# Kernel optimization log

Measured on AMD Instinct MI355X. Metric: run time of the kernel, lower is better.

Reference implementation:

```python
import jax, jax.numpy as jnp
import numpy as np

B, N = 1, 768
C_A, C_S, C_Z = 768, 384, 128
H, C_HID, N_TRANS = 16, 48, 2
INF = 1e9
PNAMES = ['attn_s_ln_g', 'attn_ada_gate_w', 'attn_ada_gate_b', 'attn_ada_skip_w',
          'wq', 'bq', 'wk', 'wv', 'z_ln_g', 'z_ln_b', 'wb', 'wg', 'wo',
          'attn_out_gate_w', 'attn_out_gate_b',
          'tr_s_ln_g', 'tr_ada_gate_w', 'tr_ada_gate_b', 'tr_ada_skip_w',
          'tr_w1', 'tr_w2', 'tr_wo', 'tr_out_gate_w', 'tr_out_gate_b']


def _ln(x, eps=1e-5):
    mu = jnp.mean(x, axis=-1, keepdims=True)
    var = jnp.mean((x - mu) ** 2, axis=-1, keepdims=True)
    return (x - mu) * jax.lax.rsqrt(var + eps)


def _adaln(a, s, s_g, gate_w, gate_b, skip_w):
    # AF3 Algorithm 26 AdaLN: a <- LN(a, no affine); s <- LN(s, scale only)
    a_ln = _ln(a)
    s_ln = _ln(s) * s_g
    return jax.nn.sigmoid(s_ln @ gate_w + gate_b) * a_ln + s_ln @ skip_w


def setup_inputs() -> dict:
    key = jax.random.key(0)
    ks = iter(jax.random.split(key, 40))
    w = lambda *sh: jax.random.normal(next(ks), sh, jnp.float32) * 0.02
    return dict(
        a=jax.random.normal(next(ks), (B, N, C_A), jnp.float32),
        s=jax.random.normal(next(ks), (B, N, C_S), jnp.float32),
        z=jax.random.normal(next(ks), (B, N, N, C_Z), jnp.float32),
        mask=jnp.ones((B, N), jnp.int32),
        attn_s_ln_g=jnp.ones((C_S,), jnp.float32),
        attn_ada_gate_w=w(C_S, C_A),
        attn_ada_gate_b=jnp.zeros((C_A,), jnp.float32),
        attn_ada_skip_w=w(C_S, C_A),
        wq=w(C_A, H * C_HID), bq=jnp.zeros((H * C_HID,), jnp.float32),
        wk=w(C_A, H * C_HID), wv=w(C_A, H * C_HID),
        z_ln_g=jnp.ones((C_Z,), jnp.float32), z_ln_b=jnp.zeros((C_Z,), jnp.float32),
        wb=w(C_Z, H), wg=w(C_A, H * C_HID), wo=w(H * C_HID, C_A),
        attn_out_gate_w=w(C_S, C_A),
        attn_out_gate_b=jnp.full((C_A,), -2.0, jnp.float32),  # AdaLN-Zero bias init -2
        tr_s_ln_g=jnp.ones((C_S,), jnp.float32),
        tr_ada_gate_w=w(C_S, C_A),
        tr_ada_gate_b=jnp.zeros((C_A,), jnp.float32),
        tr_ada_skip_w=w(C_S, C_A),
        tr_w1=w(C_A, N_TRANS * C_A), tr_w2=w(C_A, N_TRANS * C_A),
        tr_wo=w(N_TRANS * C_A, C_A),
        tr_out_gate_w=w(C_S, C_A),
        tr_out_gate_b=jnp.full((C_A,), -2.0, jnp.float32),
    )


def _block(a, s, z, maskf, p):
    # --- AttentionPairBias (AF3 Alg 24), residual ---
    a_ln = _adaln(a, s, p['attn_s_ln_g'], p['attn_ada_gate_w'],
                  p['attn_ada_gate_b'], p['attn_ada_skip_w'])
    q = (a_ln @ p['wq'] + p['bq']).reshape(B, N, H, C_HID)
    k = (a_ln @ p['wk']).reshape(B, N, H, C_HID)
    v = (a_ln @ p['wv']).reshape(B, N, H, C_HID)
    pair_bias = (_ln(z) * p['z_ln_g'] + p['z_ln_b']) @ p['wb']  # [B,N,N,H]
    logits = jnp.einsum('bqhc,bkhc->bhqk', q, k) / np.float32(np.sqrt(C_HID))
    logits = logits + jnp.moveaxis(pair_bias, -1, 1)
    logits = logits + (maskf - 1.0)[:, None, None, :] * INF  # mask over keys
    attn = jax.nn.softmax(logits, axis=-1)
    o = jnp.einsum('bhqk,bkhc->bqhc', attn, v)
    g = jax.nn.sigmoid(a_ln @ p['wg']).reshape(B, N, H, C_HID)
    o = (o * g).reshape(B, N, H * C_HID) @ p['wo']
    o = jax.nn.sigmoid(s @ p['attn_out_gate_w'] + p['attn_out_gate_b']) * o
    a = a + o
    # --- ConditionedTransitionBlock (AF3 Alg 25, SwiGLU), residual ---
    t_ln = _adaln(a, s, p['tr_s_ln_g'], p['tr_ada_gate_w'],
                  p['tr_ada_gate_b'], p['tr_ada_skip_w'])
    hid = jax.nn.silu(t_ln @ p['tr_w1']) * (t_ln @ p['tr_w2'])
    t = jax.nn.sigmoid(s @ p['tr_out_gate_w'] + p['tr_out_gate_b']) * (hid @ p['tr_wo'])
    t = t * maskf[..., None]  # _mask_trans=True
    return a + t


def reference(a, s, z, mask, attn_s_ln_g, attn_ada_gate_w, attn_ada_gate_b,
              attn_ada_skip_w, wq, bq, wk, wv, z_ln_g, z_ln_b, wb, wg, wo,
              attn_out_gate_w, attn_out_gate_b, tr_s_ln_g, tr_ada_gate_w,
              tr_ada_gate_b, tr_ada_skip_w, tr_w1, tr_w2, tr_wo,
              tr_out_gate_w, tr_out_gate_b):
    p = dict(zip(PNAMES, (attn_s_ln_g, attn_ada_gate_w, attn_ada_gate_b,
                          attn_ada_skip_w, wq, bq, wk, wv, z_ln_g, z_ln_b, wb,
                          wg, wo, attn_out_gate_w, attn_out_gate_b, tr_s_ln_g,
                          tr_ada_gate_w, tr_ada_gate_b, tr_ada_skip_w, tr_w1,
                          tr_w2, tr_wo, tr_out_gate_w, tr_out_gate_b)))
    return _block(a, s, z, mask.astype(a.dtype), p)
```

## Files before the change

kernel.cpp:

```cpp
#include <hip/hip_runtime.h>
#include <hip/hip_bf16.h>
#include <stdint.h>


typedef __bf16 bf16x8 __attribute__((ext_vector_type(8)));
typedef float  f32x4  __attribute__((ext_vector_type(4)));

#define DEVI __device__ __forceinline__

DEVI uint16_t f2b(float f){ __hip_bfloat16 h = __float2bfloat16(f); return __builtin_bit_cast(uint16_t, h); }
DEVI float    b2f(uint16_t u){ return __bfloat162float(__builtin_bit_cast(__hip_bfloat16, u)); }
DEVI float    sigm(float x){ return 1.0f/(1.0f + __expf(-x)); }

DEVI f32x4 MFMA(uint4 a, uint4 b, f32x4 c){
  return __builtin_amdgcn_mfma_f32_16x16x32_bf16(
      __builtin_bit_cast(bf16x8, a), __builtin_bit_cast(bf16x8, b), c, 0, 0, 0);
}

DEVI void glds16(const void* g, void* l){
  __builtin_amdgcn_global_load_lds(
      (const __attribute__((address_space(1))) void*)g,
      (__attribute__((address_space(3))) void*)l, 16, 0, 0);
}

constexpr size_t SZ_BT_ADA   = (size_t)1536*384*2;
constexpr size_t OFF_BT_ADA_ATTN = 0;
constexpr size_t OFF_BT_ADA_TR   = OFF_BT_ADA_ATTN + SZ_BT_ADA;
constexpr size_t OFF_BT_OUTGATE  = OFF_BT_ADA_TR   + SZ_BT_ADA;
constexpr size_t OFF_BT_QKVG     = OFF_BT_OUTGATE  + SZ_BT_ADA;
constexpr size_t OFF_BT_WO       = OFF_BT_QKVG + (size_t)3072*768*2;
constexpr size_t OFF_BT_W12      = OFF_BT_WO   + (size_t)768*768*2;
constexpr size_t OFF_BT_TRWO     = OFF_BT_W12  + (size_t)3072*768*2;
constexpr size_t OFF_WBGT        = OFF_BT_TRWO + (size_t)768*1536*2;
constexpr size_t OFF_ZCOL        = OFF_WBGT + 4096;
constexpr size_t OFF_OGB         = OFF_ZCOL + 256;
constexpr size_t OFF_SBF         = OFF_OGB + 6144;
constexpr size_t OFF_SLNA        = OFF_SBF  + (size_t)768*384*2;
constexpr size_t OFF_SLNT        = OFF_SLNA + (size_t)768*384*2;
constexpr size_t OFF_GATEOUT     = OFF_SLNT + (size_t)768*384*2;
constexpr size_t OFF_GS          = OFF_GATEOUT + (size_t)768*1536*4;
constexpr size_t OFF_GST         = OFF_GS   + (size_t)768*1536*4;
constexpr size_t OFF_ALNBF       = OFF_GST  + (size_t)768*1536*4;
constexpr size_t OFF_QKVGB       = OFF_ALNBF + (size_t)768*768*2;
constexpr size_t OFF_QP          = OFF_QKVGB + (size_t)768*3072*2;
constexpr size_t OFF_KP          = OFF_QP + (size_t)16*768*64*2;
constexpr size_t OFF_VT          = OFF_KP + (size_t)16*768*64*2;
constexpr size_t OFF_BIAS        = OFF_VT + (size_t)16*64*768*2;
constexpr size_t OFF_OBF         = OFF_BIAS + (size_t)16*768*768*2;
constexpr size_t OFF_AMID        = OFF_OBF + (size_t)768*768*2;

struct CvtArgs {
  const float* src[14];
  uint16_t*    dst[14];
  int K[14], N[14];
  int prefix[15];
};

__global__ __launch_bounds__(256) void k_cvt(CvtArgs a){
  int bid = blockIdx.x;
  int ti = 0;
  while (ti < 13 && bid >= a.prefix[ti+1]) ti++;
  int local = bid - a.prefix[ti];
  int K = a.K[ti], N = a.N[ti];
  int tN = N >> 5;
  int n0 = (local % tN) << 5, k0 = (local / tN) << 5;
  __shared__ float lds[32][33];
  const float* src = a.src[ti];
  uint16_t* dst = a.dst[ti];
  int t = threadIdx.x;
  int c = t & 31, r0 = t >> 5;
  #pragma unroll
  for (int i = 0; i < 4; i++){
    int kk = r0 + 8*i;
    lds[kk][c] = src[(size_t)(k0+kk)*N + n0 + c];
  }
  __syncthreads();
  #pragma unroll
  for (int i = 0; i < 4; i++){
    int nn = r0 + 8*i;
    dst[(size_t)(n0+nn)*K + k0 + c] = f2b(lds[c][nn]);
  }
}

__global__ __launch_bounds__(128) void k_prep(
    const float* s, const float* g_attn, const float* g_tr,
    const float* attn_ogb, const float* tr_ogb,
    const float* z_g, const float* z_b, const float* wb,
    uint16_t* s_bf, uint16_t* sln_a, uint16_t* sln_t,
    float* ogb, uint16_t* wbgt, float* zcol)
{
  int b = blockIdx.x, t = threadIdx.x;
  if (b < 768){
    const float* row = s + (size_t)b*384;
    float x0 = row[t], x1 = row[t+128], x2 = row[t+256];
    float sm = x0+x1+x2, sq = x0*x0+x1*x1+x2*x2;
    #pragma unroll
    for (int off = 32; off; off >>= 1){ sm += __shfl_xor(sm, off, 64); sq += __shfl_xor(sq, off, 64); }
    __shared__ float rs_[2], rq_[2];
    int w = t >> 6;
    if ((t & 63) == 0){ rs_[w] = sm; rq_[w] = sq; }
    __syncthreads();
    float S = rs_[0]+rs_[1], Q = rq_[0]+rq_[1];
    float mu = S * (1.f/384.f);
    float var = Q * (1.f/384.f) - mu*mu;
    float rstd = rsqrtf(var + 1e-5f);
    float xs[3] = {x0, x1, x2};
    #pragma unroll
    for (int i = 0; i < 3; i++){
      int ci = t + 128*i;
      float ln = (xs[i] - mu) * rstd;
      s_bf [(size_t)b*384 + ci] = f2b(xs[i]);
      sln_a[(size_t)b*384 + ci] = f2b(ln * g_attn[ci]);
      sln_t[(size_t)b*384 + ci] = f2b(ln * g_tr[ci]);
    }
  } else if (b == 768){
    for (int i = t; i < 1536; i += 128)
      ogb[i] = (i < 768) ? attn_ogb[i] : tr_ogb[i-768];
  } else {
    for (int i = t; i < 2048; i += 128){
      int h = i >> 7, c = i & 127;
      wbgt[i] = f2b(z_g[c] * wb[c*16 + h]);
    }
    if (t < 16){
      float cs = 0.f, cn = 0.f;
      for (int c = 0; c < 128; c++){ cs += z_g[c]*wb[c*16+t]; cn += z_b[c]*wb[c*16+t]; }
      zcol[t] = cs; zcol[16+t] = cn;
    }
  }
}

__global__ __launch_bounds__(256) void k_adaln2(
    const float* __restrict__ asrc, const float* __restrict__ gs,
    const float* __restrict__ gb, uint16_t* __restrict__ out)
{
  int b = blockIdx.x, t = threadIdx.x;
  const float* row = asrc + (size_t)b*768;
  float x0 = row[t], x1 = row[t+256], x2 = row[t+512];
  float sm = x0+x1+x2, sq = x0*x0+x1*x1+x2*x2;
  #pragma unroll
  for (int off = 32; off; off >>= 1){ sm += __shfl_xor(sm, off, 64); sq += __shfl_xor(sq, off, 64); }
  __shared__ float rs_[4], rq_[4];
  int w = t >> 6;
  if ((t & 63) == 0){ rs_[w] = sm; rq_[w] = sq; }
  __syncthreads();
  float S = rs_[0]+rs_[1]+rs_[2]+rs_[3], Q = rq_[0]+rq_[1]+rq_[2]+rq_[3];
  float mu = S*(1.f/768.f), var = Q*(1.f/768.f) - mu*mu, rstd = rsqrtf(var + 1e-5f);
  float xs[3] = {x0, x1, x2};
  #pragma unroll
  for (int i = 0; i < 3; i++){
    int c = t + 256*i;
    float g  = gs[(size_t)b*1536 + c];
    float sk = gs[(size_t)b*1536 + 768 + c];
    out[(size_t)b*768 + c] = f2b(sigm(g + gb[c]) * ((xs[i]-mu)*rstd) + sk);
  }
}

DEVI void g128_core(const uint16_t* __restrict__ A, const uint16_t* __restrict__ BT,
                    int K, int N, int m0, int n0,
                    float* outF, uint16_t* outB, int mode, const float* bias)
{
  __shared__ uint16_t As[128*64], Bs[128*64];
  int t = threadIdx.x;
  int w = t >> 6, lane = t & 63, mm = lane & 15, q = lane >> 4;
  int rowblk = (w >> 1)*64, colblk = (w & 1)*64;
  const uint16_t* gA[4]; const uint16_t* gB[4];
  uint16_t* lA[4]; uint16_t* lB[4];
  #pragma unroll
  for (int s2 = 0; s2 < 4; s2++){
    int ci = 256*w + 64*s2 + lane;
    int r = ci >> 3, c = ci & 7;
    gA[s2] = A  + (size_t)(m0 + r)*K + c*8;
    gB[s2] = BT + (size_t)(n0 + r)*K + c*8;
    lA[s2] = As + (size_t)(256*w + 64*s2)*8;
    lB[s2] = Bs + (size_t)(256*w + 64*s2)*8;
  }
  f32x4 zz = {0.f,0.f,0.f,0.f};
  f32x4 acc[4][4];
  #pragma unroll
  for (int i = 0; i < 4; i++)
    #pragma unroll
    for (int j = 0; j < 4; j++) acc[i][j] = zz;
  for (int k0 = 0; k0 < K; k0 += 64){
    __syncthreads();
    #pragma unroll
    for (int s2 = 0; s2 < 4; s2++){
      glds16(gA[s2] + k0, lA[s2]);
      glds16(gB[s2] + k0, lB[s2]);
    }
    __syncthreads();
    #pragma unroll
    for (int kc = 0; kc < 2; kc++){
      uint4 av[4], bv[4];
      #pragma unroll
      for (int i = 0; i < 4; i++)
        av[i] = *(const uint4*)&As[(rowblk + 16*i + mm)*64 + kc*32 + q*8];
      #pragma unroll
      for (int j = 0; j < 4; j++)
        bv[j] = *(const uint4*)&Bs[(colblk + 16*j + mm)*64 + kc*32 + q*8];
      #pragma unroll
      for (int i = 0; i < 4; i++)
        #pragma unroll
        for (int j = 0; j < 4; j++)
          acc[i][j] = MFMA(av[i], bv[j], acc[i][j]);
    }
  }
  #pragma unroll
  for (int i = 0; i < 4; i++){
    #pragma unroll
    for (int j = 0; j < 4; j++){
      #pragma unroll
      for (int rr = 0; rr < 4; rr++){
        int row = m0 + rowblk + 16*i + q*4 + rr;
        int col = n0 + colblk + 16*j + mm;
        float v = acc[i][j][rr];
        size_t oi = (size_t)row*N + col;
        if (mode == 0)      outF[oi] = v;
        else if (mode == 1) outB[oi] = f2b(v);
        else                outF[oi] = sigm(v + bias[col]);
      }
    }
  }
}

__global__ __launch_bounds__(256) void k_gemm128(
    const uint16_t* __restrict__ A, const uint16_t* __restrict__ BT,
    int K, int N, float* outF, uint16_t* outB, int mode, const float* bias)
{
  g128_core(A, BT, K, N, blockIdx.y*128, blockIdx.x*128, outF, outB, mode, bias);
}

__global__ __launch_bounds__(256) void k_sfused(
    const uint16_t* __restrict__ SBF, const uint16_t* __restrict__ SLNA,
    const uint16_t* __restrict__ SLNT,
    const uint16_t* __restrict__ BTo, const uint16_t* __restrict__ BTa,
    const uint16_t* __restrict__ BTt,
    float* GATEOUT, float* GS, float* GST, const float* OGB)
{
  int zi = blockIdx.z;
  const uint16_t* A  = (zi == 0) ? SBF : (zi == 1) ? SLNA : SLNT;
  const uint16_t* BT = (zi == 0) ? BTo : (zi == 1) ? BTa  : BTt;
  float* out         = (zi == 0) ? GATEOUT : (zi == 1) ? GS : GST;
  int mode           = (zi == 0) ? 2 : 0;
  g128_core(A, BT, 384, 1536, blockIdx.y*128, blockIdx.x*128, out, nullptr, mode, OGB);
}

__global__ __launch_bounds__(256) void k_gemm(
    const uint16_t* __restrict__ A, const uint16_t* __restrict__ BT,
    int M, int N, int K,
    float* outF, int mode,
    const float* gate, int gateLd, int gateOff,
    const float* resid, const int* mask)
{
  __shared__ uint16_t As[64*64], Bs[64*64];
  int t = threadIdx.x;
  int n0 = blockIdx.x*64, m0 = blockIdx.y*64;
  int w = t >> 6, lane = t & 63, mm = lane & 15, q = lane >> 4;
  int fc0 = 128*w + lane, fc1 = fc0 + 64;
  int r0 = fc0 >> 3, c0 = (fc0 & 7) ^ (r0 & 7);
  int r1 = fc1 >> 3, c1 = (fc1 & 7) ^ (r1 & 7);
  const uint16_t* gA0 = A  + (size_t)(m0 + r0)*K + c0*8;
  const uint16_t* gA1 = A  + (size_t)(m0 + r1)*K + c1*8;
  const uint16_t* gB0 = BT + (size_t)(n0 + r0)*K + c0*8;
  const uint16_t* gB1 = BT + (size_t)(n0 + r1)*K + c1*8;
  uint16_t* lA0 = As + (2*w + 0)*512;
  uint16_t* lA1 = As + (2*w + 1)*512;
  uint16_t* lB0 = Bs + (2*w + 0)*512;
  uint16_t* lB1 = Bs + (2*w + 1)*512;
  f32x4 zz = {0.f,0.f,0.f,0.f};
  f32x4 acc[4] = {zz, zz, zz, zz};
  int sw = mm & 7;
  for (int k0 = 0; k0 < K; k0 += 64){
    __syncthreads();
    glds16(gA0 + k0, lA0);
    glds16(gA1 + k0, lA1);
    glds16(gB0 + k0, lB0);
    glds16(gB1 + k0, lB1);
    __syncthreads();
    #pragma unroll
    for (int kc = 0; kc < 2; kc++){
      uint4 av = *(const uint4*)&As[(16*w + mm)*64 + ((kc*4 + q) ^ sw)*8];
      #pragma unroll
      for (int j = 0; j < 4; j++){
        uint4 bv = *(const uint4*)&Bs[(16*j + mm)*64 + ((kc*4 + q) ^ sw)*8];
        acc[j] = MFMA(av, bv, acc[j]);
      }
    }
  }
  #pragma unroll
  for (int j = 0; j < 4; j++){
    #pragma unroll
    for (int rr = 0; rr < 4; rr++){
      int row = m0 + 16*w + q*4 + rr;
      int col = n0 + 16*j + mm;
      float v = acc[j][rr];
      size_t oi = (size_t)row*N + col;
      if (mode == 5) outF[oi] = resid[oi] + gate[(size_t)row*gateLd + gateOff + col]*v;
      else {
        float mf = (float)mask[row];
        outF[oi] = resid[oi] + mf * gate[(size_t)row*gateLd + gateOff + col] * v;
      }
    }
  }
}

__global__ __launch_bounds__(256) void k_zbias(
    const float* __restrict__ z, const uint16_t* __restrict__ wbgt_g,
    const float* __restrict__ zcol, uint16_t* __restrict__ bias_g)
{
  __shared__ uint16_t zb[64*128];
  __shared__ uint16_t wbt[16*128];
  __shared__ float mu_s[64], rs_s[64];
  __shared__ uint16_t Sout[16*72];
  int t = threadIdx.x;
  size_t P0 = (size_t)blockIdx.y*768 + (size_t)blockIdx.x*64;
  ((uint4*)wbt)[t] = ((const uint4*)wbgt_g)[t];
  int p = t >> 2, qq = t & 3;
  const float4* zp = (const float4*)(z + (P0 + p)*128) + qq*8;
  float s1 = 0.f, s2 = 0.f;
  uint32_t lb[16];
  #pragma unroll
  for (int it = 0; it < 8; it++){
    float4 v = zp[it];
    s1 += v.x + v.y + v.z + v.w;
    s2 += v.x*v.x + v.y*v.y + v.z*v.z + v.w*v.w;
    lb[2*it]   = (uint32_t)f2b(v.x) | ((uint32_t)f2b(v.y) << 16);
    lb[2*it+1] = (uint32_t)f2b(v.z) | ((uint32_t)f2b(v.w) << 16);
  }
  uint4* zb4 = (uint4*)zb;
  #pragma unroll
  for (int kk = 0; kk < 4; kk++)
    zb4[p*16 + qq*4 + kk] = ((uint4*)lb)[kk];
  s1 += __shfl_xor(s1, 1, 64); s1 += __shfl_xor(s1, 2, 64);
  s2 += __shfl_xor(s2, 1, 64); s2 += __shfl_xor(s2, 2, 64);
  if (qq == 0){
    float mu = s1 * (1.f/128.f);
    mu_s[p] = mu;
    rs_s[p] = rsqrtf(s2*(1.f/128.f) - mu*mu + 1e-5f);
  }
  __syncthreads();
  int w = t >> 6, lane = t & 63, hh = lane & 15, q = lane >> 4;
  float cs = zcol[hh], cn = zcol[16 + hh];
  f32x4 acc = {0.f, 0.f, 0.f, 0.f};
  const uint4* wbt4 = (const uint4*)wbt;
  #pragma unroll
  for (int kc = 0; kc < 4; kc++){
    uint4 av = zb4[(16*w + hh)*16 + kc*4 + q];
    uint4 bv = wbt4[hh*16 + kc*4 + q];
    acc = MFMA(av, bv, acc);
  }
  #pragma unroll
  for (int rr = 0; rr < 4; rr++){
    int pl = 16*w + q*4 + rr;
    float val = rs_s[pl]*(acc[rr] - mu_s[pl]*cs) + cn;
    Sout[hh*72 + pl] = f2b(val);
  }
  __syncthreads();
  int h2 = t >> 4, p2 = (t & 15)*4;
  uint2 v2 = *(uint2*)&Sout[h2*72 + p2];
  *(uint2*)(bias_g + (size_t)h2*589824 + P0 + p2) = v2;
}

__global__ __launch_bounds__(256) void k_trans(
    const uint16_t* __restrict__ qkvg, const float* __restrict__ bq,
    uint16_t* qp, uint16_t* kp, uint16_t* vt)
{
  int h = blockIdx.y, n0 = blockIdx.x*64, t = threadIdx.x;
  __shared__ uint16_t vbuf[64*72];
  int c = t & 63, r0 = t >> 6;
  const float scale = 0.14433756729740643f;
  for (int r = r0; r < 64; r += 4){
    size_t base = (size_t)(n0 + r)*3072;
    float qv = 0.f, kv = 0.f, vv = 0.f;
    if (c < 48){
      int cc = h*48 + c;
      qv = (b2f(qkvg[base + cc]) + bq[cc]) * scale;
      kv = b2f(qkvg[base + 768 + cc]);
      vv = b2f(qkvg[base + 1536 + cc]);
    }
    size_t oi = ((size_t)h*768 + n0 + r)*64 + c;
    qp[oi] = f2b(qv);
    kp[oi] = f2b(kv);
    vbuf[c*72 + r] = f2b(vv);
  }
  __syncthreads();
  int cc = t >> 2, rb = (t & 3)*16;
  uint16_t* dst = vt + ((size_t)h*64 + cc)*768 + n0 + rb;
  *(uint4*)dst       = *(uint4*)&vbuf[cc*72 + rb];
  *(uint4*)(dst + 8) = *(uint4*)&vbuf[cc*72 + rb + 8];
}

__global__ __launch_bounds__(256) void k_flash(
    const uint16_t* __restrict__ qp, const uint16_t* __restrict__ kp,
    const uint16_t* __restrict__ vt, const uint16_t* __restrict__ bias_g,
    const uint16_t* __restrict__ qkvg, const int* __restrict__ mask,
    uint16_t* __restrict__ obf)
{
  __shared__ uint16_t Qs[64*72], Ks[64*72], Vs[64*72], Ps[64*72], Bb[64*72];
  __shared__ float mk[768];
  int t = threadIdx.x;
  int q0 = blockIdx.x*64, h = blockIdx.y;
  int w = t >> 6, lane = t & 63, mm = lane & 15, q = lane >> 4;
  {
    int row = t >> 2, c = t & 3;
    const uint4* src = (const uint4*)(qp + ((size_t)h*768 + q0 + row)*64) + c*2;
    *(uint4*)&Qs[row*72 + c*16]     = src[0];
    *(uint4*)&Qs[row*72 + c*16 + 8] = src[1];
    mk[t] = (float)mask[t]; mk[t+256] = (float)mask[t+256]; mk[t+512] = (float)mask[t+512];
  }
  f32x4 zz = {0.f,0.f,0.f,0.f};
  f32x4 o0 = zz, o1 = zz, o2 = zz;
  f32x4 m_i = {-1e30f,-1e30f,-1e30f,-1e30f};
  f32x4 l_i = zz;
  const uint16_t* bias_h = bias_g + (size_t)h*589824;
  for (int kt = 0; kt < 12; kt++){
    __syncthreads();
    {
      int row = t >> 2, c = t & 3;
      const uint4* ks = (const uint4*)(kp + ((size_t)h*768 + kt*64 + row)*64) + c*2;
      *(uint4*)&Ks[row*72 + c*16]     = ks[0];
      *(uint4*)&Ks[row*72 + c*16 + 8] = ks[1];
      const uint4* vs = (const uint4*)(vt + ((size_t)h*64 + row)*768 + kt*64) + c*2;
      *(uint4*)&Vs[row*72 + c*16]     = vs[0];
      *(uint4*)&Vs[row*72 + c*16 + 8] = vs[1];
      const uint4* bs = (const uint4*)(bias_h + (size_t)(q0 + row)*768 + kt*64) + c*2;
      *(uint4*)&Bb[row*72 + c*16]     = bs[0];
      *(uint4*)&Bb[row*72 + c*16 + 8] = bs[1];
    }
    __syncthreads();
    f32x4 s[4] = {zz, zz, zz, zz};
    #pragma unroll
    for (int kc = 0; kc < 2; kc++){
      uint4 av = *(const uint4*)&Qs[(16*w + mm)*72 + kc*32 + q*8];
      #pragma unroll
      for (int j = 0; j < 4; j++){
        uint4 bv = *(const uint4*)&Ks[(16*j + mm)*72 + kc*32 + q*8];
        s[j] = MFMA(av, bv, s[j]);
      }
    }
    #pragma unroll
    for (int j = 0; j < 4; j++){
      int scol = kt*64 + 16*j + mm;
      float mt = (mk[scol] - 1.f)*1e9f;
      int lr = 16*w + q*4;
      #pragma unroll
      for (int rr = 0; rr < 4; rr++)
        s[j][rr] += b2f(Bb[(lr+rr)*72 + 16*j + mm]) + mt;
    }
    f32x4 tm = s[0];
    #pragma unroll
    for (int j = 1; j < 4; j++)
      #pragma unroll
      for (int rr = 0; rr < 4; rr++) tm[rr] = fmaxf(tm[rr], s[j][rr]);
    #pragma unroll
    for (int off = 1; off < 16; off <<= 1)
      #pragma unroll
      for (int rr = 0; rr < 4; rr++) tm[rr] = fmaxf(tm[rr], __shfl_xor(tm[rr], off, 64));
    f32x4 mnew, alpha, rsum = zz;
    #pragma unroll
    for (int rr = 0; rr < 4; rr++){
      mnew[rr] = fmaxf(m_i[rr], tm[rr]);
      alpha[rr] = __expf(m_i[rr] - mnew[rr]);
    }
    #pragma unroll
    for (int j = 0; j < 4; j++)
      #pragma unroll
      for (int rr = 0; rr < 4; rr++){
        s[j][rr] = __expf(s[j][rr] - mnew[rr]);
        rsum[rr] += s[j][rr];
      }
    #pragma unroll
    for (int off = 1; off < 16; off <<= 1)
      #pragma unroll
      for (int rr = 0; rr < 4; rr++) rsum[rr] += __shfl_xor(rsum[rr], off, 64);
    #pragma unroll
    for (int rr = 0; rr < 4; rr++){
      l_i[rr] = l_i[rr]*alpha[rr] + rsum[rr];
      o0[rr] *= alpha[rr]; o1[rr] *= alpha[rr]; o2[rr] *= alpha[rr];
      m_i[rr] = mnew[rr];
    }
    #pragma unroll
    for (int j = 0; j < 4; j++)
      #pragma unroll
      for (int rr = 0; rr < 4; rr++)
        Ps[(16*w + q*4 + rr)*72 + 16*j + mm] = f2b(s[j][rr]);
    __syncthreads();
    #pragma unroll
    for (int kc = 0; kc < 2; kc++){
      uint4 av = *(const uint4*)&Ps[(16*w + mm)*72 + kc*32 + q*8];
      uint4 bv0 = *(const uint4*)&Vs[(mm)*72      + kc*32 + q*8];
      uint4 bv1 = *(const uint4*)&Vs[(16+mm)*72   + kc*32 + q*8];
      uint4 bv2 = *(const uint4*)&Vs[(32+mm)*72   + kc*32 + q*8];
      o0 = MFMA(av, bv0, o0);
      o1 = MFMA(av, bv1, o1);
      o2 = MFMA(av, bv2, o2);
    }
  }
  f32x4 inv;
  #pragma unroll
  for (int rr = 0; rr < 4; rr++) inv[rr] = 1.f / l_i[rr];
  #pragma unroll
  for (int j = 0; j < 3; j++){
    f32x4 ov = (j == 0) ? o0 : (j == 1) ? o1 : o2;
    int col = 16*j + mm;
    #pragma unroll
    for (int rr = 0; rr < 4; rr++){
      int row = q0 + 16*w + q*4 + rr;
      float g = b2f(qkvg[(size_t)row*3072 + 2304 + h*48 + col]);
      obf[(size_t)row*768 + h*48 + col] = f2b(ov[rr]*inv[rr]*sigm(g));
    }
  }
}

__global__ __launch_bounds__(256) void k_silu(const uint16_t* __restrict__ h12, uint16_t* __restrict__ hid){
  int idx4 = blockIdx.x*256 + threadIdx.x;
  int row = idx4 / 384;
  int c4 = (idx4 % 384)*4;
  const uint16_t* p1 = h12 + (size_t)row*3072 + c4;
  const uint16_t* p2 = p1 + 1536;
  uint16_t o[4];
  #pragma unroll
  for (int i = 0; i < 4; i++){
    float x1 = b2f(p1[i]), x2 = b2f(p2[i]);
    o[i] = f2b(x1*sigm(x1)*x2);
  }
  *(uint2*)(hid + (size_t)row*1536 + c4) = *(uint2*)o;
}

extern "C" void kernel_launch(void* const* d_in, const int* in_sizes, int n_in,
                              void* d_out, int out_size, void* d_ws, size_t ws_size,
                              hipStream_t stream)
{
  const float* a            = (const float*)d_in[0];
  const float* s            = (const float*)d_in[1];
  const float* z            = (const float*)d_in[2];
  const int*   mask         = (const int*)  d_in[3];
  const float* attn_s_ln_g  = (const float*)d_in[4];
  const float* attn_gate_w  = (const float*)d_in[5];
  const float* attn_gate_b  = (const float*)d_in[6];
  const float* attn_skip_w  = (const float*)d_in[7];
  const float* wq           = (const float*)d_in[8];
  const float* bq           = (const float*)d_in[9];
  const float* wk           = (const float*)d_in[10];
  const float* wv           = (const float*)d_in[11];
  const float* z_ln_g       = (const float*)d_in[12];
  const float* z_ln_b       = (const float*)d_in[13];
  const float* wb           = (const float*)d_in[14];
  const float* wg           = (const float*)d_in[15];
  const float* wo           = (const float*)d_in[16];
  const float* attn_og_w    = (const float*)d_in[17];
  const float* attn_og_b    = (const float*)d_in[18];
  const float* tr_s_ln_g    = (const float*)d_in[19];
  const float* tr_gate_w    = (const float*)d_in[20];
  const float* tr_gate_b    = (const float*)d_in[21];
  const float* tr_skip_w    = (const float*)d_in[22];
  const float* tr_w1        = (const float*)d_in[23];
  const float* tr_w2        = (const float*)d_in[24];
  const float* tr_wo        = (const float*)d_in[25];
  const float* tr_og_w      = (const float*)d_in[26];
  const float* tr_og_b      = (const float*)d_in[27];

  char* wsb = (char*)d_ws;
  uint16_t* BTa   = (uint16_t*)(wsb + OFF_BT_ADA_ATTN);
  uint16_t* BTt   = (uint16_t*)(wsb + OFF_BT_ADA_TR);
  uint16_t* BTo   = (uint16_t*)(wsb + OFF_BT_OUTGATE);
  uint16_t* BTq   = (uint16_t*)(wsb + OFF_BT_QKVG);
  uint16_t* BTwo  = (uint16_t*)(wsb + OFF_BT_WO);
  uint16_t* BTw12 = (uint16_t*)(wsb + OFF_BT_W12);
  uint16_t* BTtw  = (uint16_t*)(wsb + OFF_BT_TRWO);
  uint16_t* WBGT  = (uint16_t*)(wsb + OFF_WBGT);
  float*    ZCOL  = (float*)   (wsb + OFF_ZCOL);
  float*    OGB   = (float*)   (wsb + OFF_OGB);
  uint16_t* SBF   = (uint16_t*)(wsb + OFF_SBF);
  uint16_t* SLNA  = (uint16_t*)(wsb + OFF_SLNA);
  uint16_t* SLNT  = (uint16_t*)(wsb + OFF_SLNT);
  float*    GATEOUT=(float*)   (wsb + OFF_GATEOUT);
  float*    GS    = (float*)   (wsb + OFF_GS);
  float*    GST   = (float*)   (wsb + OFF_GST);
  uint16_t* ALNBF = (uint16_t*)(wsb + OFF_ALNBF);
  uint16_t* QKVGB = (uint16_t*)(wsb + OFF_QKVGB);
  uint16_t* QP    = (uint16_t*)(wsb + OFF_QP);
  uint16_t* KP    = (uint16_t*)(wsb + OFF_KP);
  uint16_t* VT    = (uint16_t*)(wsb + OFF_VT);
  uint16_t* BIASB = (uint16_t*)(wsb + OFF_BIAS);
  uint16_t* OBF   = (uint16_t*)(wsb + OFF_OBF);
  float*    AMID  = (float*)   (wsb + OFF_AMID);
  uint16_t* HIDBF = (uint16_t*)(wsb + OFF_BIAS);
  float*    OUTF  = (float*)d_out;

  CvtArgs ca;
  const float* srcs[14] = {attn_gate_w, attn_skip_w, tr_gate_w, tr_skip_w,
                           attn_og_w, tr_og_w, wq, wk, wv, wg, wo, tr_w1, tr_w2, tr_wo};
  uint16_t* dsts[14] = {BTa, BTa + (size_t)768*384, BTt, BTt + (size_t)768*384,
                        BTo, BTo + (size_t)768*384,
                        BTq, BTq + (size_t)768*768, BTq + (size_t)2*768*768, BTq + (size_t)3*768*768,
                        BTwo, BTw12, BTw12 + (size_t)1536*768, BTtw};
  int Ks[14] = {384,384,384,384,384,384, 768,768,768,768,768, 768,768, 1536};
  int Ns[14] = {768,768,768,768,768,768, 768,768,768,768,768, 1536,1536, 768};
  int tiles[14] = {288,288,288,288,288,288, 576,576,576,576,576, 1152,1152, 1152};
  int pre = 0;
  for (int i = 0; i < 14; i++){
    ca.src[i] = srcs[i]; ca.dst[i] = dsts[i]; ca.K[i] = Ks[i]; ca.N[i] = Ns[i];
    ca.prefix[i] = pre; pre += tiles[i];
  }
  ca.prefix[14] = pre;

  k_cvt<<<pre, 256, 0, stream>>>(ca);
  k_prep<<<770, 128, 0, stream>>>(s, attn_s_ln_g, tr_s_ln_g, attn_og_b, tr_og_b,
                                  z_ln_g, z_ln_b, wb, SBF, SLNA, SLNT, OGB, WBGT, ZCOL);

  k_sfused<<<dim3(12,6,3), 256, 0, stream>>>(SBF, SLNA, SLNT, BTo, BTa, BTt,
                                             GATEOUT, GS, GST, OGB);
  k_adaln2<<<768, 256, 0, stream>>>(a, GS, attn_gate_b, ALNBF);
  k_gemm128<<<dim3(24,6), 256, 0, stream>>>(ALNBF, BTq, 768, 3072,
      nullptr, QKVGB, 1, nullptr);

  k_zbias<<<dim3(12,768), 256, 0, stream>>>(z, WBGT, ZCOL, BIASB);
  k_trans<<<dim3(12,16), 256, 0, stream>>>(QKVGB, bq, QP, KP, VT);
  k_flash<<<dim3(12,16), 256, 0, stream>>>(QP, KP, VT, BIASB, QKVGB, mask, OBF);
  k_gemm<<<dim3(12,12), 256, 0, stream>>>(OBF, BTwo, 768, 768, 768,
      AMID, 5, GATEOUT, 1536, 0, a, nullptr);

  k_adaln2<<<768, 256, 0, stream>>>(AMID, GST, tr_gate_b, ALNBF);
  k_gemm128<<<dim3(24,6), 256, 0, stream>>>(ALNBF, BTw12, 768, 3072,
      nullptr, QKVGB, 1, nullptr);
  k_silu<<<1152, 256, 0, stream>>>(QKVGB, HIDBF);
  k_gemm<<<dim3(12,12), 256, 0, stream>>>(HIDBF, BTtw, 768, 768, 1536,
      OUTF, 4, GATEOUT, 1536, 768, AMID, mask);
}
```

Measured before the change: 644.5 us.

## Fuse SwiGLU into W1/W2 GEMM epilogue, merge prep into convert kernel, bf16 gates

The tr_w1 and tr_w2 weight columns are now interleaved when transposed, so a single GEMM epilogue pairs neighbouring lanes with a shuffle and writes silu(h1)*h2 directly. This removes the separate SiLU kernel and the round trip of the 3072-wide intermediate through memory. The s-prep work is folded into the weight-convert launch as extra blocks, saving one launch. The output-gate tensor is stored in bf16 instead of fp32 to cut its memory traffic, at some cost in precision.

Result: no change. 646.5 us (+0.3%).

```diff
diff --git a/kernel.cpp b/kernel.cpp
--- a/kernel.cpp
+++ b/kernel.cpp
@@ -52,72 +52,77 @@
 struct CvtArgs {
   const float* src[14];
   uint16_t*    dst[14];
-  int K[14], N[14];
+  int K[14], N[14], mul[14], add[14];
   int prefix[15];
 };
 
-__global__ __launch_bounds__(256) void k_cvt(CvtArgs a){
-  int bid = blockIdx.x;
-  int ti = 0;
-  while (ti < 13 && bid >= a.prefix[ti+1]) ti++;
-  int local = bid - a.prefix[ti];
-  int K = a.K[ti], N = a.N[ti];
-  int tN = N >> 5;
-  int n0 = (local % tN) << 5, k0 = (local / tN) << 5;
-  __shared__ float lds[32][33];
-  const float* src = a.src[ti];
-  uint16_t* dst = a.dst[ti];
-  int t = threadIdx.x;
-  int c = t & 31, r0 = t >> 5;
-  #pragma unroll
-  for (int i = 0; i < 4; i++){
-    int kk = r0 + 8*i;
-    lds[kk][c] = src[(size_t)(k0+kk)*N + n0 + c];
-  }
-  __syncthreads();
-  #pragma unroll
-  for (int i = 0; i < 4; i++){
-    int nn = r0 + 8*i;
-    dst[(size_t)(n0+nn)*K + k0 + c] = f2b(lds[c][nn]);
-  }
-}
-
-__global__ __launch_bounds__(128) void k_prep(
+__global__ __launch_bounds__(256) void k_cvt(CvtArgs a,
     const float* s, const float* g_attn, const float* g_tr,
     const float* attn_ogb, const float* tr_ogb,
     const float* z_g, const float* z_b, const float* wb,
     uint16_t* s_bf, uint16_t* sln_a, uint16_t* sln_t,
     float* ogb, uint16_t* wbgt, float* zcol)
 {
-  int b = blockIdx.x, t = threadIdx.x;
+  __shared__ float lds[32][33];
+  __shared__ float rs4[4], rq4[4];
+  int bid = blockIdx.x, t = threadIdx.x;
+  int pre = a.prefix[14];
+  if (bid < pre){
+    int ti = 0;
+    while (ti < 13 && bid >= a.prefix[ti+1]) ti++;
+    int local = bid - a.prefix[ti];
+    int K = a.K[ti], N = a.N[ti], mul = a.mul[ti], add = a.add[ti];
+    int tN = N >> 5;
+    int n0 = (local % tN) << 5, k0 = (local / tN) << 5;
+    const float* src = a.src[ti];
+    uint16_t* dst = a.dst[ti];
+    int c = t & 31, r0 = t >> 5;
+    #pragma unroll
+    for (int i = 0; i < 4; i++){
+      int kk = r0 + 8*i;
+      lds[kk][c] = src[(size_t)(k0+kk)*N + n0 + c];
+    }
+    __syncthreads();
+    #pragma unroll
+    for (int i = 0; i < 4; i++){
+      int nn = r0 + 8*i;
+      dst[(size_t)((n0+nn)*mul + add)*K + k0 + c] = f2b(lds[c][nn]);
+    }
+    return;
+  }
+  int b = bid - pre;
   if (b < 768){
     const float* row = s + (size_t)b*384;
-    float x0 = row[t], x1 = row[t+128], x2 = row[t+256];
-    float sm = x0+x1+x2, sq = x0*x0+x1*x1+x2*x2;
+    float x0 = row[t];
+    float x1 = (t < 128) ? row[256+t] : 0.f;
+    float sm = x0+x1, sq = x0*x0+x1*x1;
     #pragma unroll
     for (int off = 32; off; off >>= 1){ sm += __shfl_xor(sm, off, 64); sq += __shfl_xor(sq, off, 64); }
-    __shared__ float rs_[2], rq_[2];
     int w = t >> 6;
-    if ((t & 63) == 0){ rs_[w] = sm; rq_[w] = sq; }
-    __syncthreads();
-    float S = rs_[0]+rs_[1], Q = rq_[0]+rq_[1];
+    if ((t & 63) == 0){ rs4[w] = sm; rq4[w] = sq; }
+    __syncthreads();
+    float S = rs4[0]+rs4[1]+rs4[2]+rs4[3], Q = rq4[0]+rq4[1]+rq4[2]+rq4[3];
     float mu = S * (1.f/384.f);
     float var = Q * (1.f/384.f) - mu*mu;
     float rstd = rsqrtf(var + 1e-5f);
-    float xs[3] = {x0, x1, x2};
-    #pragma unroll
-    for (int i = 0; i < 3; i++){
-      int ci = t + 128*i;
-      float ln = (xs[i] - mu) * rstd;
-      s_bf [(size_t)b*384 + ci] = f2b(xs[i]);
+    {
+      float ln = (x0 - mu) * rstd;
+      s_bf [(size_t)b*384 + t] = f2b(x0);
+      sln_a[(size_t)b*384 + t] = f2b(ln * g_attn[t]);
+      sln_t[(size_t)b*384 + t] = f2b(ln * g_tr[t]);
+    }
+    if (t < 128){
+      int ci = 256 + t;
+      float ln = (x1 - mu) * rstd;
+      s_bf [(size_t)b*384 + ci] = f2b(x1);
       sln_a[(size_t)b*384 + ci] = f2b(ln * g_attn[ci]);
       sln_t[(size_t)b*384 + ci] = f2b(ln * g_tr[ci]);
     }
   } else if (b == 768){
-    for (int i = t; i < 1536; i += 128)
+    for (int i = t; i < 1536; i += 256)
       ogb[i] = (i < 768) ? attn_ogb[i] : tr_ogb[i-768];
   } else {
-    for (int i = t; i < 2048; i += 128){
+    for (int i = t; i < 2048; i += 256){
       int h = i >> 7, c = i & 127;
       wbgt[i] = f2b(z_g[c] * wb[c*16 + h]);
     }
@@ -213,10 +218,18 @@
         int row = m0 + rowblk + 16*i + q*4 + rr;
         int col = n0 + colblk + 16*j + mm;
         float v = acc[i][j][rr];
-        size_t oi = (size_t)row*N + col;
-        if (mode == 0)      outF[oi] = v;
-        else if (mode == 1) outB[oi] = f2b(v);
-        else                outF[oi] = sigm(v + bias[col]);
+        if (mode == 6){
+          float other = __shfl_xor(v, 1, 64);
+          if (!(mm & 1)){
+            float h1 = v, h2 = other;
+            outB[(size_t)row*(N>>1) + (col>>1)] = f2b(h1*sigm(h1)*h2);
+          }
+        } else {
+          size_t oi = (size_t)row*N + col;
+          if (mode == 0)      outF[oi] = v;
+          else if (mode == 1) outB[oi] = f2b(v);
+          else                outB[oi] = f2b(sigm(v + bias[col]));
+        }
       }
     }
   }
@@ -234,21 +247,21 @@
     const uint16_t* __restrict__ SLNT,
     const uint16_t* __restrict__ BTo, const uint16_t* __restrict__ BTa,
     const uint16_t* __restrict__ BTt,
-    float* GATEOUT, float* GS, float* GST, const float* OGB)
+    uint16_t* GATEOUT, float* GS, float* GST, const float* OGB)
 {
   int zi = blockIdx.z;
   const uint16_t* A  = (zi == 0) ? SBF : (zi == 1) ? SLNA : SLNT;
   const uint16_t* BT = (zi == 0) ? BTo : (zi == 1) ? BTa  : BTt;
-  float* out         = (zi == 0) ? GATEOUT : (zi == 1) ? GS : GST;
-  int mode           = (zi == 0) ? 2 : 0;
-  g128_core(A, BT, 384, 1536, blockIdx.y*128, blockIdx.x*128, out, nullptr, mode, OGB);
+  float* outF        = (zi == 1) ? GS : GST;
+  int mode           = (zi == 0) ? 3 : 0;
+  g128_core(A, BT, 384, 1536, blockIdx.y*128, blockIdx.x*128, outF, GATEOUT, mode, OGB);
 }
 
 __global__ __launch_bounds__(256) void k_gemm(
     const uint16_t* __restrict__ A, const uint16_t* __restrict__ BT,
     int M, int N, int K,
     float* outF, int mode,
-    const float* gate, int gateLd, int gateOff,
+    const uint16_t* gate, int gateLd, int gateOff,
     const float* resid, const int* mask)
 {
   __shared__ uint16_t As[64*64], Bs[64*64];
@@ -294,10 +307,11 @@
       int col = n0 + 16*j + mm;
       float v = acc[j][rr];
       size_t oi = (size_t)row*N + col;
-      if (mode == 5) outF[oi] = resid[oi] + gate[(size_t)row*gateLd + gateOff + col]*v;
+      float gt = b2f(gate[(size_t)row*gateLd + gateOff + col]);
+      if (mode == 5) outF[oi] = resid[oi] + gt*v;
       else {
         float mf = (float)mask[row];
-        outF[oi] = resid[oi] + mf * gate[(size_t)row*gateLd + gateOff + col] * v;
+        outF[oi] = resid[oi] + mf * gt * v;
       }
     }
   }
@@ -509,21 +523,6 @@
       obf[(size_t)row*768 + h*48 + col] = f2b(ov[rr]*inv[rr]*sigm(g));
     }
   }
-}
-
-__global__ __launch_bounds__(256) void k_silu(const uint16_t* __restrict__ h12, uint16_t* __restrict__ hid){
-  int idx4 = blockIdx.x*256 + threadIdx.x;
-  int row = idx4 / 384;
-  int c4 = (idx4 % 384)*4;
-  const uint16_t* p1 = h12 + (size_t)row*3072 + c4;
-  const uint16_t* p2 = p1 + 1536;
-  uint16_t o[4];
-  #pragma unroll
-  for (int i = 0; i < 4; i++){
-    float x1 = b2f(p1[i]), x2 = b2f(p2[i]);
-    o[i] = f2b(x1*sigm(x1)*x2);
-  }
-  *(uint2*)(hid + (size_t)row*1536 + c4) = *(uint2*)o;
 }
 
 extern "C" void kernel_launch(void* const* d_in, const int* in_sizes, int n_in,
@@ -573,7 +572,7 @@
   uint16_t* SBF   = (uint16_t*)(wsb + OFF_SBF);
   uint16_t* SLNA  = (uint16_t*)(wsb + OFF_SLNA);
   uint16_t* SLNT  = (uint16_t*)(wsb + OFF_SLNT);
-  float*    GATEOUT=(float*)   (wsb + OFF_GATEOUT);
+  uint16_t* GATEOUT=(uint16_t*)(wsb + OFF_GATEOUT);
   float*    GS    = (float*)   (wsb + OFF_GS);
   float*    GST   = (float*)   (wsb + OFF_GST);
   uint16_t* ALNBF = (uint16_t*)(wsb + OFF_ALNBF);
@@ -593,20 +592,22 @@
   uint16_t* dsts[14] = {BTa, BTa + (size_t)768*384, BTt, BTt + (size_t)768*384,
                         BTo, BTo + (size_t)768*384,
                         BTq, BTq + (size_t)768*768, BTq + (size_t)2*768*768, BTq + (size_t)3*768*768,
-                        BTwo, BTw12, BTw12 + (size_t)1536*768, BTtw};
-  int Ks[14] = {384,384,384,384,384,384, 768,768,768,768,768, 768,768, 1536};
-  int Ns[14] = {768,768,768,768,768,768, 768,768,768,768,768, 1536,1536, 768};
+                        BTwo, BTw12, BTw12, BTtw};
+  int Ks[14]   = {384,384,384,384,384,384, 768,768,768,768,768, 768,768, 1536};
+  int Ns[14]   = {768,768,768,768,768,768, 768,768,768,768,768, 1536,1536, 768};
+  int muls[14] = {1,1,1,1,1,1, 1,1,1,1,1, 2,2, 1};
+  int adds[14] = {0,0,0,0,0,0, 0,0,0,0,0, 0,1, 0};
   int tiles[14] = {288,288,288,288,288,288, 576,576,576,576,576, 1152,1152, 1152};
   int pre = 0;
   for (int i = 0; i < 14; i++){
     ca.src[i] = srcs[i]; ca.dst[i] = dsts[i]; ca.K[i] = Ks[i]; ca.N[i] = Ns[i];
+    ca.mul[i] = muls[i]; ca.add[i] = adds[i];
     ca.prefix[i] = pre; pre += tiles[i];
   }
   ca.prefix[14] = pre;
 
-  k_cvt<<<pre, 256, 0, stream>>>(ca);
-  k_prep<<<770, 128, 0, stream>>>(s, attn_s_ln_g, tr_s_ln_g, attn_og_b, tr_og_b,
-                                  z_ln_g, z_ln_b, wb, SBF, SLNA, SLNT, OGB, WBGT, ZCOL);
+  k_cvt<<<pre + 770, 256, 0, stream>>>(ca, s, attn_s_ln_g, tr_s_ln_g,
+      attn_og_b, tr_og_b, z_ln_g, z_ln_b, wb, SBF, SLNA, SLNT, OGB, WBGT, ZCOL);
 
   k_sfused<<<dim3(12,6,3), 256, 0, stream>>>(SBF, SLNA, SLNT, BTo, BTa, BTt,
                                              GATEOUT, GS, GST, OGB);
@@ -622,8 +623,7 @@
 
   k_adaln2<<<768, 256, 0, stream>>>(AMID, GST, tr_gate_b, ALNBF);
   k_gemm128<<<dim3(24,6), 256, 0, stream>>>(ALNBF, BTw12, 768, 3072,
-      nullptr, QKVGB, 1, nullptr);
-  k_silu<<<1152, 256, 0, stream>>>(QKVGB, HIDBF);
+      nullptr, HIDBF, 6, nullptr);
   k_gemm<<<dim3(12,12), 256, 0, stream>>>(HIDBF, BTtw, 768, 768, 1536,
       OUTF, 4, GATEOUT, 1536, 768, AMID, mask);
 }
```
